# Performance work log

Hardware: AMD Instinct MI355X
Metric: run time of the kernel (lower is better)

The kernel has to match this reference:

```python
import jax, jax.numpy as jnp
import numpy as np


def setup_inputs() -> dict:
    key = jax.random.key(0)
    k1, k2 = jax.random.split(key)
    x = jax.random.normal(k1, (16384, 1024), dtype=jnp.float32)
    prototypes = jax.random.normal(k2, (2048, 1024), dtype=jnp.float32)
    alpha = jnp.ones((1,), dtype=jnp.float32)
    return {"x": x, "prototypes": prototypes, "alpha": alpha}


def reference(x, prototypes, alpha):
    # distance_matrix[n,k] = (alpha + 1e-16)^2 * ||x_n - p_k||^2
    x_sq = jnp.sum(x * x, axis=-1, keepdims=True)              # [N,1]
    p_sq = jnp.sum(prototypes * prototypes, axis=-1)[None, :]  # [1,K]
    cross = jnp.einsum('nd,kd->nk', x, prototypes)             # [N,K]
    sq_dist = x_sq + p_sq - 2.0 * cross                        # [N,K]
    scale = jnp.square(alpha + 1e-16)                          # [1]
    return scale * sq_dist
```

## Files before the change

kernel.cpp:

```cpp
#include <hip/hip_runtime.h>
#include <hip/hip_fp16.h>


#define N_ROWS 16384
#define K_PROTO 2048
#define DIM 1024

#define BM 128
#define BN 128
#define BK 64
#define NT (DIM / BK)

typedef _Float16 half8 __attribute__((ext_vector_type(8)));
typedef float f32x4 __attribute__((ext_vector_type(4)));

__device__ __forceinline__ void async_copy16(void* lds_dst, const void* g_src) {
    __builtin_amdgcn_global_load_lds(
        (const __attribute__((address_space(1))) void*)g_src,
        (__attribute__((address_space(3))) void*)lds_dst,
        16, 0, 0);
}

__global__ __launch_bounds__(256) void convert_kernel(
    const float* __restrict__ x, const float* __restrict__ p,
    __half* __restrict__ xh, __half* __restrict__ ph,
    float* __restrict__ xsq, float* __restrict__ psq)
{
    int row = blockIdx.x;
    const float* src;
    __half* dst;
    float* sq;
    if (row < N_ROWS) {
        src = x + (size_t)row * DIM;
        dst = xh + (size_t)row * DIM;
        sq = xsq + row;
    } else {
        int r = row - N_ROWS;
        src = p + (size_t)r * DIM;
        dst = ph + (size_t)r * DIM;
        sq = psq + r;
    }
    int t = threadIdx.x;
    float4 v = reinterpret_cast<const float4*>(src)[t];
    float s = v.x * v.x + v.y * v.y + v.z * v.z + v.w * v.w;

    union { __half2 h[2]; uint2 u; } pk;
    pk.h[0] = __floats2half2_rn(v.x, v.y);
    pk.h[1] = __floats2half2_rn(v.z, v.w);
    reinterpret_cast<uint2*>(dst)[t] = pk.u;

    #pragma unroll
    for (int off = 32; off > 0; off >>= 1) s += __shfl_down(s, off);
    __shared__ float red[4];
    if ((t & 63) == 0) red[t >> 6] = s;
    __syncthreads();
    if (t == 0) sq[0] = red[0] + red[1] + red[2] + red[3];
}


__global__ __launch_bounds__(256, 2) void gemm_kernel(
    const __half* __restrict__ xh, const __half* __restrict__ ph,
    const float* __restrict__ xsq, const float* __restrict__ psq,
    const float* __restrict__ alpha, float* __restrict__ out)
{
    __shared__ __align__(1024) char lds[2][2 * BM * BK * 2];

    const int tid = threadIdx.x;
    const int w = tid >> 6;
    const int lane = tid & 63;
    const int wr = w >> 1;
    const int wc = w & 1;
    const int rr = lane & 15;
    const int q = lane >> 4;

    const int bm = blockIdx.x >> 4;
    const int bn = blockIdx.x & 15;

    const int c0 = w * 64 + lane;
    f32x4 acc[4][4];
    #pragma unroll
    for (int m = 0; m < 4; ++m)
        #pragma unroll
        for (int n = 0; n < 4; ++n)
            acc[m][n] = (f32x4)0.0f;

    auto stage = [&](int buf, int kt) {
        char* base = lds[buf];
        #pragma unroll
        for (int i = 0; i < 4; ++i) {
            int c = i * 256 + c0;
            int r = c >> 3;
            int ps = c & 7;
            int s = ps ^ (r & 7);
            const __half* srcA = xh + (size_t)(bm * BM + r) * DIM + kt * BK + s * 8;
            async_copy16(base + (i * 4 + w) * 1024, srcA);
        }
        #pragma unroll
        for (int i = 0; i < 4; ++i) {
            int c = i * 256 + c0;
            int r = c >> 3;
            int ps = c & 7;
            int s = ps ^ (r & 7);
            const __half* srcB = ph + (size_t)(bn * BN + r) * DIM + kt * BK + s * 8;
            async_copy16(base + 16384 + (i * 4 + w) * 1024, srcB);
        }
    };

    stage(0, 0);
    __syncthreads();

    int cur = 0;
    for (int kt = 0; kt < NT; ++kt) {
        if (kt + 1 < NT) stage(cur ^ 1, kt + 1);

        const char* Ab = lds[cur];
        const char* Bb = lds[cur] + 16384;
        #pragma unroll
        for (int kk = 0; kk < 2; ++kk) {
            half8 af[4], bf[4];
            #pragma unroll
            for (int m = 0; m < 4; ++m) {
                int row = wr * 64 + m * 16 + rr;
                int slot = kk * 4 + q;
                af[m] = *(const half8*)(Ab + row * 128 + ((slot ^ (row & 7)) * 16));
            }
            #pragma unroll
            for (int n = 0; n < 4; ++n) {
                int row = wc * 64 + n * 16 + rr;
                int slot = kk * 4 + q;
                bf[n] = *(const half8*)(Bb + row * 128 + ((slot ^ (row & 7)) * 16));
            }
            #pragma unroll
            for (int m = 0; m < 4; ++m)
                #pragma unroll
                for (int n = 0; n < 4; ++n)
                    acc[m][n] = __builtin_amdgcn_mfma_f32_16x16x32_f16(
                        af[m], bf[n], acc[m][n], 0, 0, 0);
        }
        __syncthreads();
        cur ^= 1;
    }

    const float a = alpha[0] + 1e-16f;
    const float scale = a * a;
    #pragma unroll
    for (int n = 0; n < 4; ++n) {
        int col = bn * BN + wc * 64 + n * 16 + rr;
        float pv = psq[col];
        #pragma unroll
        for (int m = 0; m < 4; ++m) {
            int rowbase = bm * BM + wr * 64 + m * 16 + q * 4;
            #pragma unroll
            for (int r = 0; r < 4; ++r) {
                int row = rowbase + r;
                out[(size_t)row * K_PROTO + col] =
                    scale * (xsq[row] + pv - 2.0f * acc[m][n][r]);
            }
        }
    }
}

__global__ __launch_bounds__(256) void fallback_kernel(
    const float* __restrict__ x, const float* __restrict__ p,
    const float* __restrict__ alpha, float* __restrict__ out)
{
    __shared__ float xs[DIM];
    int n = blockIdx.x;
    int t = threadIdx.x;
    reinterpret_cast<float4*>(xs)[t] = reinterpret_cast<const float4*>(x + (size_t)n * DIM)[t];
    __syncthreads();
    const float a = alpha[0] + 1e-16f;
    const float scale = a * a;
    for (int j = 0; j < K_PROTO / 256; ++j) {
        int k = j * 256 + t;
        const float4* pr = reinterpret_cast<const float4*>(p + (size_t)k * DIM);
        float s = 0.0f;
        #pragma unroll 8
        for (int d4 = 0; d4 < DIM / 4; ++d4) {
            float4 pv = pr[d4];
            float dx = xs[d4 * 4 + 0] - pv.x;
            float dy = xs[d4 * 4 + 1] - pv.y;
            float dz = xs[d4 * 4 + 2] - pv.z;
            float dw = xs[d4 * 4 + 3] - pv.w;
            s += dx * dx + dy * dy + dz * dz + dw * dw;
        }
        out[(size_t)n * K_PROTO + k] = scale * s;
    }
}

extern "C" void kernel_launch(void* const* d_in, const int* in_sizes, int n_in,
                              void* d_out, int out_size, void* d_ws, size_t ws_size,
                              hipStream_t stream) {
    const float* x = (const float*)d_in[0];
    const float* p = (const float*)d_in[1];
    const float* alpha = (const float*)d_in[2];
    float* out = (float*)d_out;

    const size_t XH_BYTES = (size_t)N_ROWS * DIM * sizeof(__half);
    const size_t PH_BYTES = (size_t)K_PROTO * DIM * sizeof(__half);
    const size_t NEED = XH_BYTES + PH_BYTES +
                        (size_t)(N_ROWS + K_PROTO) * sizeof(float);

    if (ws_size < NEED) {
        fallback_kernel<<<dim3(N_ROWS), dim3(256), 0, stream>>>(x, p, alpha, out);
        return;
    }

    char* w = (char*)d_ws;
    __half* xh = (__half*)w;
    __half* ph = (__half*)(w + XH_BYTES);
    float* xsq = (float*)(w + XH_BYTES + PH_BYTES);
    float* psq = (float*)(w + XH_BYTES + PH_BYTES + N_ROWS * sizeof(float));

    convert_kernel<<<dim3(N_ROWS + K_PROTO), dim3(256), 0, stream>>>(
        x, p, xh, ph, xsq, psq);
    gemm_kernel<<<dim3((N_ROWS / BM) * (K_PROTO / BN)), dim3(256), 0, stream>>>(
        xh, ph, xsq, psq, alpha, out);
}
```

Baseline: 260.8 us.

## Use 256x256 tiles with 8 waves and phased quarter-tile pipelined MFMA schedule

Replaces the 128x128, 4-wave GEMM with a 256x256, 8-wave kernel using 128KB of dynamic LDS double buffering. Each k-step is split into four half-tile async loads interleaved with four MFMA phases, using barriers, explicit waitcnt and s_setprio, in the style of an 8-wave ping-pong schedule. Block indices are also swizzled for L2 locality. The aim is more data reuse per LDS byte and better overlap of global loads with MFMA. The cost is a large register footprint (128 accumulator floats) and fewer blocks in flight, leaving only 256 blocks.

```diff
diff --git a/kernel.cpp b/kernel.cpp
--- a/kernel.cpp
+++ b/kernel.cpp
@@ -6,10 +6,11 @@
 #define K_PROTO 2048
 #define DIM 1024
 
-#define BM 128
-#define BN 128
+#define BM 256
+#define BN 256
 #define BK 64
 #define NT (DIM / BK)
+#define NHT (4 * NT)
 
 typedef _Float16 half8 __attribute__((ext_vector_type(8)));
 typedef float f32x4 __attribute__((ext_vector_type(4)));
@@ -58,101 +59,152 @@
 }
 
 
-__global__ __launch_bounds__(256, 2) void gemm_kernel(
+#define LDA(mo)                                                                      \
+    do {                                                                             \
+        _Pragma("unroll")                                                            \
+        for (int m_ = 0; m_ < 4; ++m_) {                                             \
+            const int row_ = wm * 128 + ((mo) + m_) * 16 + rr;                       \
+            _Pragma("unroll")                                                        \
+            for (int kk_ = 0; kk_ < 2; ++kk_)                                        \
+                Af[m_][kk_] = *(const half8*)(Ab + row_ * 128 +                      \
+                                   (((kk_ * 4 + lq) ^ (row_ & 7)) << 4));            \
+        }                                                                            \
+    } while (0)
+
+#define LDB(n)                                                                       \
+    do {                                                                             \
+        const int row_ = wn * 64 + (n) * 16 + rr;                                    \
+        _Pragma("unroll")                                                            \
+        for (int kk_ = 0; kk_ < 2; ++kk_)                                            \
+            Bf[n][kk_] = *(const half8*)(Bb + row_ * 128 +                           \
+                               (((kk_ * 4 + lq) ^ (row_ & 7)) << 4));                \
+    } while (0)
+
+#define MMA8(mo, n0)                                                                 \
+    do {                                                                             \
+        _Pragma("unroll")                                                            \
+        for (int m_ = 0; m_ < 4; ++m_)                                               \
+            _Pragma("unroll")                                                        \
+            for (int n_ = 0; n_ < 2; ++n_)                                           \
+                _Pragma("unroll")                                                    \
+                for (int kk_ = 0; kk_ < 2; ++kk_)                                    \
+                    acc[(mo) + m_][(n0) + n_] =                                      \
+                        __builtin_amdgcn_mfma_f32_16x16x32_f16(                      \
+                            Af[m_][kk_], Bf[(n0) + n_][kk_],                         \
+                            acc[(mo) + m_][(n0) + n_], 0, 0, 0);                     \
+    } while (0)
+
+#define PHASE_MID()                                                                  \
+    __builtin_amdgcn_s_barrier();                                                    \
+    asm volatile("s_waitcnt lgkmcnt(0)" ::: "memory");                               \
+    __builtin_amdgcn_s_setprio(1)
+
+#define PHASE_END()                                                                  \
+    __builtin_amdgcn_s_setprio(0);                                                   \
+    __builtin_amdgcn_s_barrier()
+
+__global__ __launch_bounds__(512, 2) void gemm8_kernel(
     const __half* __restrict__ xh, const __half* __restrict__ ph,
     const float* __restrict__ xsq, const float* __restrict__ psq,
     const float* __restrict__ alpha, float* __restrict__ out)
 {
-    __shared__ __align__(1024) char lds[2][2 * BM * BK * 2];
+    extern __shared__ char lds[];
 
     const int tid = threadIdx.x;
-    const int w = tid >> 6;
-    const int lane = tid & 63;
-    const int wr = w >> 1;
-    const int wc = w & 1;
-    const int rr = lane & 15;
-    const int q = lane >> 4;
-
-    const int bm = blockIdx.x >> 4;
-    const int bn = blockIdx.x & 15;
-
-    const int c0 = w * 64 + lane;
-    f32x4 acc[4][4];
-    #pragma unroll
-    for (int m = 0; m < 4; ++m)
+    const int w = tid >> 6, lane = tid & 63;
+    const int wm = w >> 2, wn = w & 3;
+    const int rr = lane & 15, lq = lane >> 4;
+
+    const int bid = blockIdx.x;
+    const int swz = (bid & 7) * 64 + (bid >> 3);
+    const int bm = swz >> 3, bn = swz & 7;
+
+    const __half* Abase = xh + (size_t)bm * BM * DIM;
+    const __half* Bbase = ph + (size_t)bn * BN * DIM;
+
+    f32x4 acc[8][4];
+    #pragma unroll
+    for (int m = 0; m < 8; ++m)
         #pragma unroll
         for (int n = 0; n < 4; ++n)
             acc[m][n] = (f32x4)0.0f;
 
-    auto stage = [&](int buf, int kt) {
-        char* base = lds[buf];
+    auto stage_ht = [&](int s) {
+        if (s >= NHT) return;
+        const int T = s >> 2, j = s & 3;
+        char* buf = lds + (size_t)(T & 1) * 65536;
+        const bool isA = (j >= 2);
+        const int rowoff = (j & 1) << 7;
+        const __half* gb = isA ? Abase : Bbase;
+        char* region = buf + (isA ? 0 : 32768) + rowoff * 128;
         #pragma unroll
-        for (int i = 0; i < 4; ++i) {
-            int c = i * 256 + c0;
-            int r = c >> 3;
-            int ps = c & 7;
-            int s = ps ^ (r & 7);
-            const __half* srcA = xh + (size_t)(bm * BM + r) * DIM + kt * BK + s * 8;
-            async_copy16(base + (i * 4 + w) * 1024, srcA);
-        }
-        #pragma unroll
-        for (int i = 0; i < 4; ++i) {
-            int c = i * 256 + c0;
-            int r = c >> 3;
-            int ps = c & 7;
-            int s = ps ^ (r & 7);
-            const __half* srcB = ph + (size_t)(bn * BN + r) * DIM + kt * BK + s * 8;
-            async_copy16(base + 16384 + (i * 4 + w) * 1024, srcB);
+        for (int i = 0; i < 2; ++i) {
+            const int c = i * 512 + tid;
+            const int r = c >> 3;
+            const int sl = (c & 7) ^ (r & 7);
+            async_copy16(region + c * 16,
+                         gb + (size_t)(rowoff + r) * DIM + T * BK + sl * 8);
         }
     };
 
-    stage(0, 0);
-    __syncthreads();
-
-    int cur = 0;
-    for (int kt = 0; kt < NT; ++kt) {
-        if (kt + 1 < NT) stage(cur ^ 1, kt + 1);
-
-        const char* Ab = lds[cur];
-        const char* Bb = lds[cur] + 16384;
-        #pragma unroll
-        for (int kk = 0; kk < 2; ++kk) {
-            half8 af[4], bf[4];
-            #pragma unroll
-            for (int m = 0; m < 4; ++m) {
-                int row = wr * 64 + m * 16 + rr;
-                int slot = kk * 4 + q;
-                af[m] = *(const half8*)(Ab + row * 128 + ((slot ^ (row & 7)) * 16));
-            }
-            #pragma unroll
-            for (int n = 0; n < 4; ++n) {
-                int row = wc * 64 + n * 16 + rr;
-                int slot = kk * 4 + q;
-                bf[n] = *(const half8*)(Bb + row * 128 + ((slot ^ (row & 7)) * 16));
-            }
-            #pragma unroll
-            for (int m = 0; m < 4; ++m)
-                #pragma unroll
-                for (int n = 0; n < 4; ++n)
-                    acc[m][n] = __builtin_amdgcn_mfma_f32_16x16x32_f16(
-                        af[m], bf[n], acc[m][n], 0, 0, 0);
-        }
-        __syncthreads();
-        cur ^= 1;
+    half8 Af[4][2], Bf[4][2];
+    const char *Ab, *Bb;
+
+    #pragma unroll
+    for (int s = 0; s < 6; ++s) stage_ht(s);
+    asm volatile("s_waitcnt vmcnt(4)" ::: "memory");
+    __builtin_amdgcn_s_barrier();
+
+    for (int t = 0; t < NT; ++t) {
+        const char* base = lds + (size_t)(t & 1) * 65536;
+        Ab = base; Bb = base + 32768;
+        const int p = t * 4;
+
+        LDA(0); LDB(0); LDB(1);
+        stage_ht(p + 6);
+        PHASE_MID();
+        MMA8(0, 0);
+        PHASE_END();
+
+        LDB(2); LDB(3);
+        stage_ht(p + 7);
+        PHASE_MID();
+        MMA8(0, 2);
+        PHASE_END();
+
+        LDA(4);
+        stage_ht(p + 8);
+        PHASE_MID();
+        MMA8(4, 2);
+        PHASE_END();
+
+        stage_ht(p + 9);
+        __builtin_amdgcn_s_barrier();
+        asm volatile("s_waitcnt lgkmcnt(0)" ::: "memory");
+        __builtin_amdgcn_s_setprio(1);
+        MMA8(4, 0);
+        __builtin_amdgcn_s_setprio(0);
+        if (t == NT - 2)
+            asm volatile("s_waitcnt vmcnt(0)" ::: "memory");
+        else if (t < NT - 2)
+            asm volatile("s_waitcnt vmcnt(4)" ::: "memory");
+        __builtin_amdgcn_s_barrier();
     }
 
     const float a = alpha[0] + 1e-16f;
     const float scale = a * a;
+    const int row0 = bm * BM + wm * 128 + lq * 4;
+    const int col0 = bn * BN + wn * 64 + rr;
     #pragma unroll
     for (int n = 0; n < 4; ++n) {
-        int col = bn * BN + wc * 64 + n * 16 + rr;
-        float pv = psq[col];
+        const int col = col0 + n * 16;
+        const float pv = psq[col];
         #pragma unroll
-        for (int m = 0; m < 4; ++m) {
-            int rowbase = bm * BM + wr * 64 + m * 16 + q * 4;
+        for (int m = 0; m < 8; ++m) {
+            const int rbase = row0 + m * 16;
             #pragma unroll
             for (int r = 0; r < 4; ++r) {
-                int row = rowbase + r;
+                const int row = rbase + r;
                 out[(size_t)row * K_PROTO + col] =
                     scale * (xsq[row] + pv - 2.0f * acc[m][n][r]);
             }
@@ -214,6 +266,6 @@
 
     convert_kernel<<<dim3(N_ROWS + K_PROTO), dim3(256), 0, stream>>>(
         x, p, xh, ph, xsq, psq);
-    gemm_kernel<<<dim3((N_ROWS / BM) * (K_PROTO / BN)), dim3(256), 0, stream>>>(
+    gemm8_kernel<<<dim3((N_ROWS / BM) * (K_PROTO / BN)), dim3(512), 131072, stream>>>(
         xh, ph, xsq, psq, alpha, out);
 }
```

Result: slower. 278.7 us (+6.9%).

## Load B fragments directly into registers, stage only A in LDS, swizzle blocks

Applied to the files above, without the earlier changes.

B (prototype) fragments now go straight from global memory into registers with double-buffered register sets, and only the A tile is staged in LDS. This halves LDS use and LDS read traffic, and the occupancy hint rises to 3 blocks per CU. Other changes: the k-loop is unrolled by two with a fixed buffer pattern, block IDs are remapped so concurrently running blocks share rows of x for better L2 reuse, and the epilogue reads xsq as vectors. The cost is more VGPR pressure and uncoalesced 16-byte global loads for B, whose latency is only covered by the one-stage register prefetch.

```diff
diff --git a/kernel.cpp b/kernel.cpp
--- a/kernel.cpp
+++ b/kernel.cpp
@@ -58,25 +58,55 @@
 }
 
 
-__global__ __launch_bounds__(256, 2) void gemm_kernel(
+#define LOADB(dst, kt)                                                            \
+    do {                                                                          \
+        _Pragma("unroll")                                                         \
+        for (int n_ = 0; n_ < 4; ++n_) {                                          \
+            const int row_ = bn * BN + wn * 64 + n_ * 16 + rr;                    \
+            _Pragma("unroll")                                                     \
+            for (int kk_ = 0; kk_ < 2; ++kk_)                                     \
+                dst[n_][kk_] = *(const half8*)(ph + (size_t)row_ * DIM +          \
+                                   (kt) * BK + (kk_ * 4 + lq) * 8);               \
+        }                                                                         \
+    } while (0)
+
+#define COMPUTE(buf, Bc)                                                          \
+    do {                                                                          \
+        const char* Ab = lds[buf];                                                \
+        _Pragma("unroll")                                                         \
+        for (int kk_ = 0; kk_ < 2; ++kk_) {                                       \
+            half8 af[4];                                                          \
+            _Pragma("unroll")                                                     \
+            for (int m_ = 0; m_ < 4; ++m_) {                                      \
+                const int row_ = wm * 64 + m_ * 16 + rr;                          \
+                af[m_] = *(const half8*)(Ab + row_ * 128 +                        \
+                             (((kk_ * 4 + lq) ^ (row_ & 7)) << 4));               \
+            }                                                                     \
+            _Pragma("unroll")                                                     \
+            for (int m_ = 0; m_ < 4; ++m_)                                        \
+                _Pragma("unroll")                                                 \
+                for (int n_ = 0; n_ < 4; ++n_)                                    \
+                    acc[m_][n_] = __builtin_amdgcn_mfma_f32_16x16x32_f16(         \
+                        af[m_], Bc[n_][kk_], acc[m_][n_], 0, 0, 0);               \
+        }                                                                         \
+    } while (0)
+
+__global__ __launch_bounds__(256, 3) void gemm_kernel(
     const __half* __restrict__ xh, const __half* __restrict__ ph,
     const float* __restrict__ xsq, const float* __restrict__ psq,
     const float* __restrict__ alpha, float* __restrict__ out)
 {
-    __shared__ __align__(1024) char lds[2][2 * BM * BK * 2];
+    __shared__ __align__(1024) char lds[2][BM * BK * 2];
 
     const int tid = threadIdx.x;
-    const int w = tid >> 6;
-    const int lane = tid & 63;
-    const int wr = w >> 1;
-    const int wc = w & 1;
-    const int rr = lane & 15;
-    const int q = lane >> 4;
-
-    const int bm = blockIdx.x >> 4;
-    const int bn = blockIdx.x & 15;
-
-    const int c0 = w * 64 + lane;
+    const int w = tid >> 6, lane = tid & 63;
+    const int wm = w >> 1, wn = w & 1;
+    const int rr = lane & 15, lq = lane >> 4;
+
+    const int bid = blockIdx.x;
+    const int swz = (bid & 7) * 256 + (bid >> 3);
+    const int bm = swz >> 4, bn = swz & 15;
+
     f32x4 acc[4][4];
     #pragma unroll
     for (int m = 0; m < 4; ++m)
@@ -88,73 +118,55 @@
         char* base = lds[buf];
         #pragma unroll
         for (int i = 0; i < 4; ++i) {
-            int c = i * 256 + c0;
-            int r = c >> 3;
-            int ps = c & 7;
-            int s = ps ^ (r & 7);
-            const __half* srcA = xh + (size_t)(bm * BM + r) * DIM + kt * BK + s * 8;
-            async_copy16(base + (i * 4 + w) * 1024, srcA);
-        }
-        #pragma unroll
-        for (int i = 0; i < 4; ++i) {
-            int c = i * 256 + c0;
-            int r = c >> 3;
-            int ps = c & 7;
-            int s = ps ^ (r & 7);
-            const __half* srcB = ph + (size_t)(bn * BN + r) * DIM + kt * BK + s * 8;
-            async_copy16(base + 16384 + (i * 4 + w) * 1024, srcB);
+            const int c = i * 256 + tid;
+            const int r = c >> 3;
+            const int sl = (c & 7) ^ (r & 7);
+            async_copy16(base + c * 16,
+                         xh + (size_t)(bm * BM + r) * DIM + kt * BK + sl * 8);
         }
     };
 
+    half8 BA[4][2], BB[4][2];
+
     stage(0, 0);
+    LOADB(BA, 0);
     __syncthreads();
 
-    int cur = 0;
-    for (int kt = 0; kt < NT; ++kt) {
-        if (kt + 1 < NT) stage(cur ^ 1, kt + 1);
-
-        const char* Ab = lds[cur];
-        const char* Bb = lds[cur] + 16384;
-        #pragma unroll
-        for (int kk = 0; kk < 2; ++kk) {
-            half8 af[4], bf[4];
-            #pragma unroll
-            for (int m = 0; m < 4; ++m) {
-                int row = wr * 64 + m * 16 + rr;
-                int slot = kk * 4 + q;
-                af[m] = *(const half8*)(Ab + row * 128 + ((slot ^ (row & 7)) * 16));
-            }
-            #pragma unroll
-            for (int n = 0; n < 4; ++n) {
-                int row = wc * 64 + n * 16 + rr;
-                int slot = kk * 4 + q;
-                bf[n] = *(const half8*)(Bb + row * 128 + ((slot ^ (row & 7)) * 16));
-            }
-            #pragma unroll
-            for (int m = 0; m < 4; ++m)
-                #pragma unroll
-                for (int n = 0; n < 4; ++n)
-                    acc[m][n] = __builtin_amdgcn_mfma_f32_16x16x32_f16(
-                        af[m], bf[n], acc[m][n], 0, 0, 0);
-        }
+    for (int t = 0; t < NT; t += 2) {
+        stage(1, t + 1);
+        LOADB(BB, t + 1);
+        COMPUTE(0, BA);
         __syncthreads();
-        cur ^= 1;
+
+        if (t + 2 < NT) {
+            stage(0, t + 2);
+            LOADB(BA, t + 2);
+        }
+        COMPUTE(1, BB);
+        __syncthreads();
     }
 
     const float a = alpha[0] + 1e-16f;
     const float scale = a * a;
+    const int row0 = bm * BM + wm * 64 + lq * 4;
+    const int col0 = bn * BN + wn * 64 + rr;
+    float4 xs4[4];
+    #pragma unroll
+    for (int m = 0; m < 4; ++m)
+        xs4[m] = *reinterpret_cast<const float4*>(xsq + row0 + m * 16);
     #pragma unroll
     for (int n = 0; n < 4; ++n) {
-        int col = bn * BN + wc * 64 + n * 16 + rr;
-        float pv = psq[col];
+        const int col = col0 + n * 16;
+        const float pv = psq[col];
         #pragma unroll
         for (int m = 0; m < 4; ++m) {
-            int rowbase = bm * BM + wr * 64 + m * 16 + q * 4;
+            const int rbase = row0 + m * 16;
             #pragma unroll
             for (int r = 0; r < 4; ++r) {
-                int row = rowbase + r;
-                out[(size_t)row * K_PROTO + col] =
-                    scale * (xsq[row] + pv - 2.0f * acc[m][n][r]);
+                const float xv = (r == 0) ? xs4[m].x : (r == 1) ? xs4[m].y
+                               : (r == 2) ? xs4[m].z : xs4[m].w;
+                out[(size_t)(rbase + r) * K_PROTO + col] =
+                    scale * (xv + pv - 2.0f * acc[m][n][r]);
             }
         }
     }
```

Result: slower. 326.8 us (+25.3%).
